# Kernel optimization log

Measured on AMD Instinct MI355X. Metric: run time of the kernel, lower is better.

The kernel has to match this reference:

```python
import jax, jax.numpy as jnp
import numpy as np
from jax import lax

B, T, U, V = 4, 256, 64, 1024   # batch, enc frames, max target len, vocab (blank=0)
F, H, HD, J = 80, 512, 512, 512  # feat dim, enc dim, dec dim, joint dim
NEG = -1e30


def setup_inputs() -> dict:
    key = jax.random.key(0)
    ks = jax.random.split(key, 10)
    inputs = jax.random.normal(ks[0], (B, T, F), dtype=jnp.float32)
    targets = jax.random.randint(ks[1], (B, U), 1, V, dtype=jnp.int32)  # labels exclude blank=0
    input_lengths = jax.random.randint(ks[2], (B,), T // 2, T + 1, dtype=jnp.int32)
    target_lengths = jax.random.randint(ks[3], (B,), U // 2, U + 1, dtype=jnp.int32)
    s = 0.02
    W_enc = jax.random.normal(ks[4], (F, H), dtype=jnp.float32) * s
    emb = jax.random.normal(ks[5], (V, HD), dtype=jnp.float32) * s
    W_jenc = jax.random.normal(ks[6], (H, J), dtype=jnp.float32) * s
    W_jdec = jax.random.normal(ks[7], (HD, J), dtype=jnp.float32) * s
    b_j = jnp.zeros((J,), dtype=jnp.float32)
    W_out = jax.random.normal(ks[8], (J, V), dtype=jnp.float32) * s
    b_out = jnp.zeros((V,), dtype=jnp.float32)
    return {"inputs": inputs, "W_enc": W_enc, "emb": emb, "W_jenc": W_jenc,
            "W_jdec": W_jdec, "b_j": b_j, "W_out": W_out, "b_out": b_out,
            "targets": targets, "input_lengths": input_lengths,
            "target_lengths": target_lengths}


def rnnt_loss(log_probs, targets, in_lens, tgt_lens):
    """RNN-T loss (blank=0, 'gather' variant: gather blank/label lps, then DP).
    log_probs: (B,T,U+1,V) log-softmaxed joint. Returns mean loss over batch."""
    Bq, Tq, U1, _ = log_probs.shape
    Uq = U1 - 1
    blank_lp = log_probs[..., 0]                                    # (B,T,U+1)
    lbl_lp = jnp.take_along_axis(
        log_probs[:, :, :Uq, :],
        jnp.broadcast_to(targets[:, None, :, None], (Bq, Tq, Uq, 1)),
        axis=3)[..., 0]                                             # (B,T,U)
    u_idx = jnp.arange(Uq)
    lbl_lp = jnp.where(u_idx[None, None, :] < tgt_lens[:, None, None], lbl_lp, NEG)

    def row(a, py):
        # a: (B,U+1) = alpha_prev + blank emission; py: (B,U) label lps this frame
        def step(c, x):
            a_u, py_prev = x
            c = jnp.logaddexp(a_u, c + py_prev)
            return c, c
        c0 = a[:, 0]
        _, rest = lax.scan(step, c0, (a[:, 1:].T, py.T))            # (U,B)
        return jnp.concatenate([c0[:, None], rest.T], axis=1)      # (B,U+1)

    # t=0 row: alpha[0,u] = cumsum of label lps at frame 0
    alpha0 = jnp.concatenate(
        [jnp.zeros((Bq, 1), log_probs.dtype),
         jnp.cumsum(lbl_lp[:, 0, :], axis=1)], axis=1)              # (B,U+1)

    def tstep(alpha_prev, x):
        blank_prev, py_t = x
        alpha = row(alpha_prev + blank_prev, py_t)
        return alpha, alpha

    xs = (jnp.swapaxes(blank_lp[:, :-1, :], 0, 1),                  # (T-1,B,U+1)
          jnp.swapaxes(lbl_lp[:, 1:, :], 0, 1))                    # (T-1,B,U)
    _, rest = lax.scan(tstep, alpha0, xs)
    alphas = jnp.concatenate([alpha0[None], rest], axis=0)          # (T,B,U+1)

    b = jnp.arange(Bq)
    t_last = in_lens - 1
    a_fin = alphas[t_last, b, tgt_lens] + blank_lp[b, t_last, tgt_lens]
    return -jnp.mean(a_fin)


def reference(inputs, W_enc, emb, W_jenc, W_jdec, b_j, W_out, b_out,
              targets, input_lengths, target_lengths):
    enc = inputs @ W_enc                                            # (B,T,H) encoder
    padded = jnp.concatenate(
        [jnp.zeros((targets.shape[0], 1), targets.dtype), targets], axis=1)
    dec = emb[padded]                                               # (B,U+1,HD) decoder
    e = enc @ W_jenc                                                # (B,T,J)
    d = dec @ W_jdec                                                # (B,U+1,J)
    h = jnp.tanh(e[:, :, None, :] + d[:, None, :, :] + b_j)        # (B,T,U+1,J)
    logits = h @ W_out + b_out                                      # (B,T,U+1,V)
    log_probs = jax.nn.log_softmax(logits, axis=-1)
    return rnnt_loss(log_probs, targets, input_lengths, target_lengths)
```

## Files before the change

### kernel.cpp

```cpp
#include <hip/hip_runtime.h>
#include <stdint.h>

#define NEGF (-1e30f)

typedef unsigned short ushort_t;
typedef unsigned char uchar_t;
typedef __attribute__((ext_vector_type(2))) long v2i64;
typedef __attribute__((ext_vector_type(4))) float f32x4;

constexpr int cB = 4, cT = 256, cU = 64, cU1 = 65, cV = 1024, cF = 80, cH = 512, cJ = 512;
constexpr int cM = cB * cT * cU1;
constexpr int cTU = cT * cU1;
constexpr float LOG2E = 1.4426950408889634f;

__device__ __forceinline__ float tanh_fast(float x){
  float t = x * x;
  float num = x * (27.f + t);
  float den = fmaf(9.f, t, 27.f);
  float r = num * __builtin_amdgcn_rcpf(den);
  return fminf(1.f, fmaxf(-1.f, r));
}

__device__ __forceinline__ float logadd2(float x, float y){
  float m = fmaxf(x, y);
  return m + __builtin_amdgcn_logf(1.f + __builtin_amdgcn_exp2f(-fabsf(x - y)));
}

__device__ __forceinline__ float wshr1(float x){
  return __int_as_float(__builtin_amdgcn_mov_dpp(__float_as_int(x),
                                                 0x138, 0xF, 0xF, true));
}

__device__ __forceinline__ int pk8(float a, float b, float c, float d){
  int v = __builtin_amdgcn_cvt_pk_fp8_f32(a, b, 0, false);
  v = __builtin_amdgcn_cvt_pk_fp8_f32(c, d, v, true);
  return v;
}

__global__ __launch_bounds__(256) void k_pre(
    const float* __restrict__ inputs,
    const float* __restrict__ W_enc, const float* __restrict__ W_jenc,
    const float* __restrict__ emb, const int* __restrict__ targets,
    const float* __restrict__ W_jdec, const float* __restrict__ b_j,
    float* __restrict__ dmatb, float* __restrict__ e,
    const float* __restrict__ W_out, uchar_t* __restrict__ WTf8,
    float* __restrict__ S, float* __restrict__ out_loss)
{
  __shared__ float sA[4][512];
  __shared__ float sIn[4][80];
  int bid = blockIdx.x;
  int tid = threadIdx.x;

  if (bid < 256){
    int m0 = bid * 4;
    for (int i = tid; i < 320; i += 256)
      sIn[i / 80][i % 80] = inputs[m0 * 80 + i];
    __syncthreads();
    int c0 = tid, c1 = tid + 256;
    float a00 = 0.f, a01 = 0.f, a10 = 0.f, a11 = 0.f;
    float a20 = 0.f, a21 = 0.f, a30 = 0.f, a31 = 0.f;
#pragma unroll 8
    for (int k = 0; k < 80; k++){
      float w0 = W_enc[(size_t)k * 512 + c0];
      float w1 = W_enc[(size_t)k * 512 + c1];
      a00 = fmaf(sIn[0][k], w0, a00); a01 = fmaf(sIn[0][k], w1, a01);
      a10 = fmaf(sIn[1][k], w0, a10); a11 = fmaf(sIn[1][k], w1, a11);
      a20 = fmaf(sIn[2][k], w0, a20); a21 = fmaf(sIn[2][k], w1, a21);
      a30 = fmaf(sIn[3][k], w0, a30); a31 = fmaf(sIn[3][k], w1, a31);
    }
    sA[0][c0] = a00; sA[0][c1] = a01;
    sA[1][c0] = a10; sA[1][c1] = a11;
    sA[2][c0] = a20; sA[2][c1] = a21;
    sA[3][c0] = a30; sA[3][c1] = a31;
    __syncthreads();
    float b00 = 0.f, b01 = 0.f, b10 = 0.f, b11 = 0.f;
    float b20 = 0.f, b21 = 0.f, b30 = 0.f, b31 = 0.f;
#pragma unroll 8
    for (int k = 0; k < 512; k++){
      float w0 = W_jenc[(size_t)k * 512 + c0];
      float w1 = W_jenc[(size_t)k * 512 + c1];
      b00 = fmaf(sA[0][k], w0, b00); b01 = fmaf(sA[0][k], w1, b01);
      b10 = fmaf(sA[1][k], w0, b10); b11 = fmaf(sA[1][k], w1, b11);
      b20 = fmaf(sA[2][k], w0, b20); b21 = fmaf(sA[2][k], w1, b21);
      b30 = fmaf(sA[3][k], w0, b30); b31 = fmaf(sA[3][k], w1, b31);
    }
    e[(size_t)(m0 + 0) * 512 + c0] = b00; e[(size_t)(m0 + 0) * 512 + c1] = b01;
    e[(size_t)(m0 + 1) * 512 + c0] = b10; e[(size_t)(m0 + 1) * 512 + c1] = b11;
    e[(size_t)(m0 + 2) * 512 + c0] = b20; e[(size_t)(m0 + 2) * 512 + c1] = b21;
    e[(size_t)(m0 + 3) * 512 + c0] = b30; e[(size_t)(m0 + 3) * 512 + c1] = b31;
  } else if (bid < 386){
    int id = bid - 256;
    int bx = id & 1, by = id >> 1;
    int m0 = by * 4;
    int col = bx * 256 + tid;
    for (int i = tid; i < 4 * 512; i += 256){
      int r = i >> 9, c = i & 511;
      int row = m0 + r;
      int b = row / cU1, u = row % cU1;
      int src = (u == 0) ? 0 : targets[b * cU + (u - 1)];
      sA[r][c] = emb[(size_t)src * cH + c];
    }
    __syncthreads();
    float a0 = 0.f, a1 = 0.f, a2 = 0.f, a3 = 0.f;
#pragma unroll 8
    for (int k = 0; k < 512; k++){
      float bv = W_jdec[(size_t)k * cJ + col];
      a0 = fmaf(sA[0][k], bv, a0);
      a1 = fmaf(sA[1][k], bv, a1);
      a2 = fmaf(sA[2][k], bv, a2);
      a3 = fmaf(sA[3][k], bv, a3);
    }
    float bb = b_j[col];
    dmatb[(size_t)(m0 + 0) * cJ + col] = a0 + bb;
    dmatb[(size_t)(m0 + 1) * cJ + col] = a1 + bb;
    dmatb[(size_t)(m0 + 2) * cJ + col] = a2 + bb;
    dmatb[(size_t)(m0 + 3) * cJ + col] = a3 + bb;
  } else if (bid < 418){
    int id = bid - 386;
    int bn = id & 3, ksp = id >> 2;
    int lane = tid & 63, nth = tid >> 6;
    int c16 = lane & 15, quad = lane >> 4;
    int jA = ksp * 64 + quad * 8;
#pragma unroll
    for (int i = 0; i < 4; i++){
      int nt16 = nth * 4 + i;
      int n = bn * 256 + nt16 * 16 + c16;
      unsigned int p[4];
#pragma unroll
      for (int h = 0; h < 4; h++){
        int j0 = jA + (h >> 1) * 32 + (h & 1) * 4;
        float w0 = W_out[(size_t)(j0 + 0) * cV + n] * 32.f;
        float w1 = W_out[(size_t)(j0 + 1) * cV + n] * 32.f;
        float w2 = W_out[(size_t)(j0 + 2) * cV + n] * 32.f;
        float w3 = W_out[(size_t)(j0 + 3) * cV + n] * 32.f;
        p[h] = (unsigned)pk8(w0, w1, w2, w3);
      }
      uint4 pack; pack.x = p[0]; pack.y = p[1]; pack.z = p[2]; pack.w = p[3];
      *(uint4*)(WTf8 + (((size_t)(bn * 8 + ksp) * 16 + nt16) * 64 + lane) * 16) = pack;
    }
  } else {
    int i = (bid - 418) * 1024 + tid * 4;
    float4 z; z.x = 0.f; z.y = 0.f; z.z = 0.f; z.w = 0.f;
    *(float4*)(S + i) = z;
    if (bid == 418 && tid == 0) out_loss[0] = 0.f;
  }
}

__global__ __launch_bounds__(256) void k_hf(const float* __restrict__ e,
                                            const float* __restrict__ dmatb,
                                            uchar_t* __restrict__ Hbf8){
  __shared__ uchar_t sH[16 * 520];
  int tid = threadIdx.x;
  int wid = tid >> 6, lane = tid & 63;
  int c16 = lane & 15, quad = lane >> 4;
  int bm = blockIdx.x;
  int bu = bm >> 1, thalf = bm & 1;
  int b = bu / cU1;
  int t0 = thalf * 128;

  float dj[8];
  const float4* dp = (const float4*)(dmatb + (size_t)bu * cJ + lane * 8);
  float4 dA = dp[0], dB = dp[1];
  dj[0] = dA.x; dj[1] = dA.y; dj[2] = dA.z; dj[3] = dA.w;
  dj[4] = dB.x; dj[5] = dB.y; dj[6] = dB.z; dj[7] = dB.w;

  const float* erow0 = e + ((size_t)(b * cT + t0)) * cJ + lane * 8;
  uchar_t* outb = Hbf8 + (size_t)bm * 65536 + lane * 16;

  for (int mg = 0; mg < 8; mg++){
#pragma unroll
    for (int rr = 0; rr < 4; rr++){
      int rloc = wid * 4 + rr;
      const float* ep = erow0 + ((size_t)(mg * 16 + rloc)) * cJ;
      float4 e0 = *(const float4*)ep;
      float4 e1 = *(const float4*)(ep + 4);
      int v0 = pk8(tanh_fast(e0.x + dj[0]), tanh_fast(e0.y + dj[1]),
                   tanh_fast(e0.z + dj[2]), tanh_fast(e0.w + dj[3]));
      int v1 = pk8(tanh_fast(e1.x + dj[4]), tanh_fast(e1.y + dj[5]),
                   tanh_fast(e1.z + dj[6]), tanh_fast(e1.w + dj[7]));
      uint2 pk; pk.x = (unsigned)v0; pk.y = (unsigned)v1;
      *(uint2*)(sH + rloc * 520 + lane * 8) = pk;
    }
    __syncthreads();
#pragma unroll
    for (int q = 0; q < 2; q++){
      int ksp = wid * 2 + q;
      uint2 lo = *(const uint2*)(sH + c16 * 520 + ksp * 64 + quad * 8);
      uint2 hi = *(const uint2*)(sH + c16 * 520 + ksp * 64 + 32 + quad * 8);
      uint4 pack; pack.x = lo.x; pack.y = lo.y; pack.z = hi.x; pack.w = hi.y;
      *(uint4*)(outb + ((size_t)ksp * 8 + mg) * 1024) = pack;
    }
    __syncthreads();
  }
}

__global__ __launch_bounds__(256, 3) void k_joint(
    const uchar_t* __restrict__ Hbf8, const uchar_t* __restrict__ WTf8,
    const float* __restrict__ b_out, const int* __restrict__ targets,
    float* __restrict__ S,
    float* __restrict__ blank_g, float* __restrict__ lbl_g)
{
  __shared__ float redP[2][128][19];

  int tid = threadIdx.x;
  int wid = tid >> 6, lane = tid & 63;
  int quad = lane >> 4, c16 = lane & 15;
  int wm = wid & 1, wn = wid >> 1;
  int bid = blockIdx.x;
  int bm = ((bid >> 6) << 3) + (bid & 7);
  int bn = (bid >> 3) & 7;
  int bu = bm >> 1, thalf = bm & 1;
  int b = bu / cU1, u = bu - b * cU1;
  int tg = (u < cU) ? targets[b * cU + u] : -1;
  int lin0 = bu * cT + thalf * 128;

  f32x4 acc[4][4];
#pragma unroll
  for (int i = 0; i < 4; i++)
#pragma unroll
    for (int j = 0; j < 4; j++)
      acc[i][j] = (f32x4){0.f, 0.f, 0.f, 0.f};

  const uchar_t* aP = Hbf8 + (size_t)bm * 65536 + (wm * 4) * 1024 + lane * 16;
  const uchar_t* bP = WTf8 + (size_t)(bn >> 1) * 131072 + ((bn & 1) * 8 + wn * 4) * 1024 + lane * 16;

  v2i64 afX[4], bfX[4], afY[4], bfY[4];
#pragma unroll
  for (int mt = 0; mt < 4; mt++) afX[mt] = *(const v2i64*)(aP + mt * 1024);
#pragma unroll
  for (int nt = 0; nt < 4; nt++) bfX[nt] = *(const v2i64*)(bP + nt * 1024);

#pragma unroll
  for (int k2 = 0; k2 < 4; k2++){
    {
      size_t kY = (size_t)(2 * k2 + 1);
#pragma unroll
      for (int mt = 0; mt < 4; mt++) afY[mt] = *(const v2i64*)(aP + kY * 8192 + mt * 1024);
#pragma unroll
      for (int nt = 0; nt < 4; nt++) bfY[nt] = *(const v2i64*)(bP + kY * 16384 + nt * 1024);
    }
#pragma unroll
    for (int h = 0; h < 2; h++)
#pragma unroll
      for (int mt = 0; mt < 4; mt++)
#pragma unroll
        for (int nt = 0; nt < 4; nt++)
          acc[mt][nt] = __builtin_amdgcn_mfma_f32_16x16x32_fp8_fp8(afX[mt][h], bfX[nt][h], acc[mt][nt], 0, 0, 0);
    if (k2 < 3){
      size_t kX = (size_t)(2 * k2 + 2);
#pragma unroll
      for (int mt = 0; mt < 4; mt++) afX[mt] = *(const v2i64*)(aP + kX * 8192 + mt * 1024);
#pragma unroll
      for (int nt = 0; nt < 4; nt++) bfX[nt] = *(const v2i64*)(bP + kX * 16384 + nt * 1024);
    }
#pragma unroll
    for (int h = 0; h < 2; h++)
#pragma unroll
      for (int mt = 0; mt < 4; mt++)
#pragma unroll
        for (int nt = 0; nt < 4; nt++)
          acc[mt][nt] = __builtin_amdgcn_mfma_f32_16x16x32_fp8_fp8(afY[mt][h], bfY[nt][h], acc[mt][nt], 0, 0, 0);
  }

  float bv[4];
#pragma unroll
  for (int nt = 0; nt < 4; nt++) bv[nt] = b_out[bn * 128 + (wn * 4 + nt) * 16 + c16] * LOG2E;

  bool ownL = (tg >= 0) && ((tg >> 7) == bn) && (((tg >> 6) & 1) == wn);
  int ntO = (tg >> 4) & 3;
  int tgc = tg & 15;
  const float descale2 = LOG2E / 32.f;

#pragma unroll
  for (int mt = 0; mt < 4; mt++){
#pragma unroll
    for (int r = 0; r < 4; r++){
      int rl = wm * 64 + mt * 16 + quad * 4 + r;
      float l[4];
#pragma unroll
      for (int nt = 0; nt < 4; nt++) l[nt] = fmaf(acc[mt][nt][r], descale2, bv[nt]);
      if (bn == 0 && wn == 0 && c16 == 0) blank_g[lin0 + rl] = l[0];
      if (ownL && c16 == tgc){
        float v = l[0];
#pragma unroll
        for (int k = 1; k < 4; k++) v = (ntO == k) ? l[k] : v;
        lbl_g[lin0 + rl] = v;
      }
      redP[wn][rl][c16] = __builtin_amdgcn_exp2f(l[0]) + __builtin_amdgcn_exp2f(l[1])
                        + __builtin_amdgcn_exp2f(l[2]) + __builtin_amdgcn_exp2f(l[3]);
    }
  }
  __syncthreads();
  if (tid < 128){
    float a = 0.f;
#pragma unroll
    for (int j = 0; j < 16; j++) a += redP[0][tid][j] + redP[1][tid][j];
    atomicAdd(&S[lin0 + tid], a);
  }
}

__global__ __launch_bounds__(256) void k_dp(
    const float* __restrict__ S, const float* __restrict__ blank_g,
    const float* __restrict__ lbl_g,
    const int* __restrict__ in_len, const int* __restrict__ tgt_len,
    float* __restrict__ out)
{
  constexpr int G = 16;
  __shared__ float sbb[cTU];
  __shared__ float slb[cTU];
  __shared__ float sS[256];
  __shared__ float cC0[G * 64], cC1[G * 64], cC2[G * 64];
  __shared__ float cOA[G * 64], cOB[G * 64];
  int tid = threadIdx.x;
  int b = blockIdx.x;
  int tl  = tgt_len[b];
  size_t base = (size_t)b * cTU;
  for (int i = tid; i < cTU / 4; i += 256){
    int row = i >> 6;
    if (row > tl) continue;
    float4 sv = ((const float4*)(S + base))[i];
    float4 bvv = ((const float4*)(blank_g + base))[i];
    float4 ls;
    ls.x = __builtin_amdgcn_logf(sv.x); ls.y = __builtin_amdgcn_logf(sv.y);
    ls.z = __builtin_amdgcn_logf(sv.z); ls.w = __builtin_amdgcn_logf(sv.w);
    float4 bo;
    bo.x = bvv.x - ls.x; bo.y = bvv.y - ls.y;
    bo.z = bvv.z - ls.z; bo.w = bvv.w - ls.w;
    ((float4*)sbb)[i] = bo;
    float4 lo;
    if (row < tl){
      float4 lv = ((const float4*)(lbl_g + base))[i];
      lo.x = lv.x - ls.x; lo.y = lv.y - ls.y;
      lo.z = lv.z - ls.z; lo.w = lv.w - ls.w;
    } else {
      lo.x = NEGF; lo.y = NEGF; lo.z = NEGF; lo.w = NEGF;
    }
    ((float4*)slb)[i] = lo;
  }
  __syncthreads();

  int til = in_len[b] - 1;
  bool cap64 = (tl == 64);
  int u = tid;
  bool isTL = (u == tl);
  float fb = (tid < 64) ? sbb[(u << 8) + til] : 0.f;

  int need = til + tl;
  if (cap64 && til + 62 > need) need = til + 62;
  int gmax = (need >> 1) + 2;
  if (gmax > 159) gmax = 159;
  int nph = (gmax + G - 1) / G;

  float A = (u == 0) ? 0.f : NEGF;
  float res = 0.f;

  auto ld = [&](const float* p, int i, bool ok) -> float {
    float x = p[i & 255];
    return (ok & ((unsigned)i < 256u)) ? x : NEGF;
  };

  for (int p = 0; p < nph; p++){
    for (int w = tid; w < G * 64; w += 256){
      int gg = w >> 6, uu = w & 63;
      int g = p * G + gg;
      int i0 = 2 * g - uu;
      bool v1 = (uu >= 1), v2 = (uu >= 2);
      const float* pbu  = sbb + (uu << 8);
      const float* pbu1 = sbb + ((v1 ? uu - 1 : 0) << 8);
      const float* plu1 = slb + ((v1 ? uu - 1 : 0) << 8);
      const float* plu2 = slb + ((v2 ? uu - 2 : 0) << 8);
      float o0 = ld(pbu,  i0,     true);
      float o1 = ld(pbu,  i0 + 1, true);
      float o2 = ld(plu1, i0 + 1, v1);
      float o3 = ld(pbu1, i0 + 1, v1);
      float o4 = ld(plu1, i0 + 2, v1);
      float o5 = ld(plu2, i0 + 2, v2);
      cC0[w] = o0 + o1;
      cC1[w] = logadd2(o2 + o1, o3 + o4);
      cC2[w] = o5 + o4;
      cOA[w] = o0;
      cOB[w] = o2;
    }
    __syncthreads();
    if (tid < 64){
      float c0v = cC0[u], c1v = cC1[u], c2v = cC2[u];
      float oAv = cOA[u], oBv = cOB[u];
#pragma unroll
      for (int gg = 0; gg < G; gg++){
        int g = p * G + gg;
        int nx = (gg + 1 < G) ? ((gg + 1) << 6) + u : (gg << 6) + u;
        float nc0 = cC0[nx], nc1 = cC1[nx], nc2 = cC2[nx];
        float noA = cOA[nx], noB = cOB[nx];
        if (g < gmax){
          float up1 = wshr1(A);
          float up2 = wshr1(up1);
          int i0 = 2 * g - u;
          float Amid = logadd2(A + oAv, up1 + oBv);
          bool tv1 = ((unsigned)(i0 + 1) < 256u);
          Amid = tv1 ? Amid : NEGF;
          float a0 = A + c0v, a1 = up1 + c1v, a2 = up2 + c2v;
          float m3 = fmaxf(fmaxf(a0, a1), a2);
          float s3 = __builtin_amdgcn_exp2f(a0 - m3) + __builtin_amdgcn_exp2f(a1 - m3)
                   + __builtin_amdgcn_exp2f(a2 - m3);
          float Anew = m3 + __builtin_amdgcn_logf(s3);
          bool tv2 = ((unsigned)(i0 + 2) < 256u);
          Anew = tv2 ? Anew : NEGF;
          if (isTL && (i0 + 1) == til) res = Amid + fb;
          if (isTL && (i0 + 2) == til) res = Anew + fb;
          if (u == 63){
            if (tv1) sS[i0 + 1] = Amid;
            if (tv2) sS[i0 + 2] = Anew;
          }
          A = Anew;
        }
        c0v = nc0; c1v = nc1; c2v = nc2; oAv = noA; oBv = noB;
      }
    }
    __syncthreads();
  }

  if (tid >= 64) return;

  if (cap64){
    const float* pb64 = sbb + (64 << 8);
    const float* pl63 = slb + (63 << 8);
    float A64 = sS[0] + pl63[0];
    for (int t = 1; t <= til; t++)
      A64 = logadd2(A64 + pb64[t - 1], sS[t] + pl63[t]);
    if (u == 0) res = A64 + pb64[til];
  }

  res += __shfl_xor(res, 1, 64);
  res += __shfl_xor(res, 2, 64);
  res += __shfl_xor(res, 4, 64);
  res += __shfl_xor(res, 8, 64);
  res += __shfl_xor(res, 16, 64);
  res += __shfl_xor(res, 32, 64);
  if (u == 0) atomicAdd(out, -0.17328679513998632f * res);
}

extern "C" void kernel_launch(void* const* d_in, const int* in_sizes, int n_in,
                              void* d_out, int out_size, void* d_ws, size_t ws_size,
                              hipStream_t stream)
{
  (void)in_sizes; (void)n_in; (void)out_size; (void)ws_size;
  const float* inputs = (const float*)d_in[0];
  const float* W_enc  = (const float*)d_in[1];
  const float* emb    = (const float*)d_in[2];
  const float* W_jenc = (const float*)d_in[3];
  const float* W_jdec = (const float*)d_in[4];
  const float* b_j    = (const float*)d_in[5];
  const float* W_out  = (const float*)d_in[6];
  const float* b_out  = (const float*)d_in[7];
  const int* targets  = (const int*)d_in[8];
  const int* in_len   = (const int*)d_in[9];
  const int* tgt_len  = (const int*)d_in[10];

  char* w = (char*)d_ws;
  auto alloc = [&](size_t bytes){ char* p = w; w += (bytes + 255) & ~(size_t)255; return p; };
  float* e       = (float*)alloc((size_t)1024 * 512 * 4);
  float* dmatb   = (float*)alloc((size_t)260 * 512 * 4);
  float* blank_g = (float*)alloc((size_t)cM * 4);
  float* lbl_g   = (float*)alloc((size_t)cM * 4);
  float* S       = (float*)alloc((size_t)cM * 4);
  uchar_t* Hbf8  = (uchar_t*)alloc((size_t)520 * 65536);
  uchar_t* WTf8  = (uchar_t*)alloc((size_t)4 * 131072);

  k_pre<<<483, 256, 0, stream>>>(inputs, W_enc, W_jenc, emb, targets, W_jdec, b_j,
                                 dmatb, e, W_out, WTf8, S, (float*)d_out);
  k_hf<<<520, 256, 0, stream>>>(e, dmatb, Hbf8);
  k_joint<<<4160, 256, 0, stream>>>(Hbf8, WTf8, b_out, targets, S, blank_g, lbl_g);
  k_dp<<<4, 256, 0, stream>>>(S, blank_g, lbl_g, in_len, tgt_len, (float*)d_out);
}
```

Before: 202.9 us.

## Switch joint GEMM to 32x32x16 FP8 MFMA with matching operand layouts

Replaces the 16x16x32 FP8 MFMA tiles in the joint GEMM with 32x32x16 FP8 MFMA tiles, giving each wave a 2x2 grid of 32x32 accumulators instead of 4x4 grid of 16x16. The pre-packing of W_out and the tanh/pack kernel are rewritten to emit operands in the 32x32 fragment layout, and the epilogue row mapping and shared reduction buffer are widened to 32 columns. The aim is fewer MFMA issues and fewer fragment loads per K step. The cost is a larger LDS reduction buffer, more staging in k_hf, and a different accumulator register layout that could affect occupancy.

```diff
diff --git a/kernel.cpp b/kernel.cpp
--- a/kernel.cpp
+++ b/kernel.cpp
@@ -7,6 +7,7 @@
 typedef unsigned char uchar_t;
 typedef __attribute__((ext_vector_type(2))) long v2i64;
 typedef __attribute__((ext_vector_type(4))) float f32x4;
+typedef __attribute__((ext_vector_type(16))) float f32x16;
 
 constexpr int cB = 4, cT = 256, cU = 64, cU1 = 65, cV = 1024, cF = 80, cH = 512, cJ = 512;
 constexpr int cM = cB * cT * cU1;
@@ -117,26 +118,30 @@
     dmatb[(size_t)(m0 + 3) * cJ + col] = a3 + bb;
   } else if (bid < 418){
     int id = bid - 386;
-    int bn = id & 3, ksp = id >> 2;
-    int lane = tid & 63, nth = tid >> 6;
-    int c16 = lane & 15, quad = lane >> 4;
-    int jA = ksp * 64 + quad * 8;
-#pragma unroll
-    for (int i = 0; i < 4; i++){
-      int nt16 = nth * 4 + i;
-      int n = bn * 256 + nt16 * 16 + c16;
-      unsigned int p[4];
-#pragma unroll
-      for (int h = 0; h < 4; h++){
-        int j0 = jA + (h >> 1) * 32 + (h & 1) * 4;
-        float w0 = W_out[(size_t)(j0 + 0) * cV + n] * 32.f;
-        float w1 = W_out[(size_t)(j0 + 1) * cV + n] * 32.f;
-        float w2 = W_out[(size_t)(j0 + 2) * cV + n] * 32.f;
-        float w3 = W_out[(size_t)(j0 + 3) * cV + n] * 32.f;
-        p[h] = (unsigned)pk8(w0, w1, w2, w3);
+    int bn = id & 7, jq = id >> 3;
+    int lane = tid & 63, nt32 = tid >> 6;
+    int c32 = lane & 31, kh = lane >> 5;
+    int col = bn * 128 + nt32 * 32 + c32;
+#pragma unroll
+    for (int jj = 0; jj < 4; jj++){
+      int j = jq * 4 + jj;
+      unsigned p[4];
+#pragma unroll
+      for (int h = 0; h < 2; h++){
+        int k0 = 32 * j + 16 * h + kh * 8;
+        float w0 = W_out[(size_t)(k0 + 0) * cV + col] * 32.f;
+        float w1 = W_out[(size_t)(k0 + 1) * cV + col] * 32.f;
+        float w2 = W_out[(size_t)(k0 + 2) * cV + col] * 32.f;
+        float w3 = W_out[(size_t)(k0 + 3) * cV + col] * 32.f;
+        float w4 = W_out[(size_t)(k0 + 4) * cV + col] * 32.f;
+        float w5 = W_out[(size_t)(k0 + 5) * cV + col] * 32.f;
+        float w6 = W_out[(size_t)(k0 + 6) * cV + col] * 32.f;
+        float w7 = W_out[(size_t)(k0 + 7) * cV + col] * 32.f;
+        p[h * 2 + 0] = (unsigned)pk8(w0, w1, w2, w3);
+        p[h * 2 + 1] = (unsigned)pk8(w4, w5, w6, w7);
       }
       uint4 pack; pack.x = p[0]; pack.y = p[1]; pack.z = p[2]; pack.w = p[3];
-      *(uint4*)(WTf8 + (((size_t)(bn * 8 + ksp) * 16 + nt16) * 64 + lane) * 16) = pack;
+      *(uint4*)(WTf8 + (((size_t)(bn * 4 + nt32) * 16 + j) * 64 + lane) * 16) = pack;
     }
   } else {
     int i = (bid - 418) * 1024 + tid * 4;
@@ -149,10 +154,10 @@
 __global__ __launch_bounds__(256) void k_hf(const float* __restrict__ e,
                                             const float* __restrict__ dmatb,
                                             uchar_t* __restrict__ Hbf8){
-  __shared__ uchar_t sH[16 * 520];
+  __shared__ uchar_t sH[32 * 520];
   int tid = threadIdx.x;
   int wid = tid >> 6, lane = tid & 63;
-  int c16 = lane & 15, quad = lane >> 4;
+  int c32 = lane & 31, kh = lane >> 5;
   int bm = blockIdx.x;
   int bu = bm >> 1, thalf = bm & 1;
   int b = bu / cU1;
@@ -167,11 +172,11 @@
   const float* erow0 = e + ((size_t)(b * cT + t0)) * cJ + lane * 8;
   uchar_t* outb = Hbf8 + (size_t)bm * 65536 + lane * 16;
 
-  for (int mg = 0; mg < 8; mg++){
-#pragma unroll
-    for (int rr = 0; rr < 4; rr++){
-      int rloc = wid * 4 + rr;
-      const float* ep = erow0 + ((size_t)(mg * 16 + rloc)) * cJ;
+  for (int g = 0; g < 4; g++){
+#pragma unroll
+    for (int rr = 0; rr < 8; rr++){
+      int rloc = wid * 8 + rr;
+      const float* ep = erow0 + ((size_t)(g * 32 + rloc)) * cJ;
       float4 e0 = *(const float4*)ep;
       float4 e1 = *(const float4*)(ep + 4);
       int v0 = pk8(tanh_fast(e0.x + dj[0]), tanh_fast(e0.y + dj[1]),
@@ -183,12 +188,13 @@
     }
     __syncthreads();
 #pragma unroll
-    for (int q = 0; q < 2; q++){
-      int ksp = wid * 2 + q;
-      uint2 lo = *(const uint2*)(sH + c16 * 520 + ksp * 64 + quad * 8);
-      uint2 hi = *(const uint2*)(sH + c16 * 520 + ksp * 64 + 32 + quad * 8);
+    for (int jj = 0; jj < 4; jj++){
+      int j = wid * 4 + jj;
+      const uchar_t* src = sH + c32 * 520 + 32 * j + kh * 8;
+      uint2 lo = *(const uint2*)(src);
+      uint2 hi = *(const uint2*)(src + 16);
       uint4 pack; pack.x = lo.x; pack.y = lo.y; pack.z = hi.x; pack.w = hi.y;
-      *(uint4*)(outb + ((size_t)ksp * 8 + mg) * 1024) = pack;
+      *(uint4*)(outb + ((size_t)(g * 16 + j)) * 1024) = pack;
     }
     __syncthreads();
   }
@@ -200,11 +206,11 @@
     float* __restrict__ S,
     float* __restrict__ blank_g, float* __restrict__ lbl_g)
 {
-  __shared__ float redP[2][128][19];
+  __shared__ float redP[2][128][33];
 
   int tid = threadIdx.x;
   int wid = tid >> 6, lane = tid & 63;
-  int quad = lane >> 4, c16 = lane & 15;
+  int c32 = lane & 31, kh = lane >> 5;
   int wm = wid & 1, wn = wid >> 1;
   int bid = blockIdx.x;
   int bm = ((bid >> 6) << 3) + (bid & 7);
@@ -214,87 +220,81 @@
   int tg = (u < cU) ? targets[b * cU + u] : -1;
   int lin0 = bu * cT + thalf * 128;
 
-  f32x4 acc[4][4];
-#pragma unroll
-  for (int i = 0; i < 4; i++)
-#pragma unroll
-    for (int j = 0; j < 4; j++)
-      acc[i][j] = (f32x4){0.f, 0.f, 0.f, 0.f};
-
-  const uchar_t* aP = Hbf8 + (size_t)bm * 65536 + (wm * 4) * 1024 + lane * 16;
-  const uchar_t* bP = WTf8 + (size_t)(bn >> 1) * 131072 + ((bn & 1) * 8 + wn * 4) * 1024 + lane * 16;
-
-  v2i64 afX[4], bfX[4], afY[4], bfY[4];
-#pragma unroll
-  for (int mt = 0; mt < 4; mt++) afX[mt] = *(const v2i64*)(aP + mt * 1024);
-#pragma unroll
-  for (int nt = 0; nt < 4; nt++) bfX[nt] = *(const v2i64*)(bP + nt * 1024);
-
-#pragma unroll
-  for (int k2 = 0; k2 < 4; k2++){
+  f32x16 acc[2][2];
+#pragma unroll
+  for (int i = 0; i < 2; i++)
+#pragma unroll
+    for (int j = 0; j < 2; j++)
+#pragma unroll
+      for (int r = 0; r < 16; r++) acc[i][j][r] = 0.f;
+
+  const uchar_t* aP = Hbf8 + (size_t)bm * 65536 + (size_t)wm * 32768 + lane * 16;
+  const uchar_t* bP = WTf8 + (size_t)bn * 65536 + (size_t)wn * 32768 + lane * 16;
+
+  v2i64 afX[2], bfX[2], afY[2], bfY[2];
+#pragma unroll
+  for (int mt = 0; mt < 2; mt++) afX[mt] = *(const v2i64*)(aP + mt * 16384);
+#pragma unroll
+  for (int nt = 0; nt < 2; nt++) bfX[nt] = *(const v2i64*)(bP + nt * 16384);
+
+#pragma unroll
+  for (int j2 = 0; j2 < 8; j2++){
     {
-      size_t kY = (size_t)(2 * k2 + 1);
-#pragma unroll
-      for (int mt = 0; mt < 4; mt++) afY[mt] = *(const v2i64*)(aP + kY * 8192 + mt * 1024);
-#pragma unroll
-      for (int nt = 0; nt < 4; nt++) bfY[nt] = *(const v2i64*)(bP + kY * 16384 + nt * 1024);
+      size_t jY = (size_t)(2 * j2 + 1) * 1024;
+      afY[0] = *(const v2i64*)(aP + jY);
+      afY[1] = *(const v2i64*)(aP + 16384 + jY);
+      bfY[0] = *(const v2i64*)(bP + jY);
+      bfY[1] = *(const v2i64*)(bP + 16384 + jY);
     }
 #pragma unroll
     for (int h = 0; h < 2; h++)
 #pragma unroll
-      for (int mt = 0; mt < 4; mt++)
-#pragma unroll
-        for (int nt = 0; nt < 4; nt++)
-          acc[mt][nt] = __builtin_amdgcn_mfma_f32_16x16x32_fp8_fp8(afX[mt][h], bfX[nt][h], acc[mt][nt], 0, 0, 0);
-    if (k2 < 3){
-      size_t kX = (size_t)(2 * k2 + 2);
-#pragma unroll
-      for (int mt = 0; mt < 4; mt++) afX[mt] = *(const v2i64*)(aP + kX * 8192 + mt * 1024);
-#pragma unroll
-      for (int nt = 0; nt < 4; nt++) bfX[nt] = *(const v2i64*)(bP + kX * 16384 + nt * 1024);
+      for (int mt = 0; mt < 2; mt++)
+#pragma unroll
+        for (int nt = 0; nt < 2; nt++)
+          acc[mt][nt] = __builtin_amdgcn_mfma_f32_32x32x16_fp8_fp8(afX[mt][h], bfX[nt][h], acc[mt][nt], 0, 0, 0);
+    if (j2 < 7){
+      size_t jX = (size_t)(2 * j2 + 2) * 1024;
+      afX[0] = *(const v2i64*)(aP + jX);
+      afX[1] = *(const v2i64*)(aP + 16384 + jX);
+      bfX[0] = *(const v2i64*)(bP + jX);
+      bfX[1] = *(const v2i64*)(bP + 16384 + jX);
     }
 #pragma unroll
     for (int h = 0; h < 2; h++)
 #pragma unroll
-      for (int mt = 0; mt < 4; mt++)
-#pragma unroll
-        for (int nt = 0; nt < 4; nt++)
-          acc[mt][nt] = __builtin_amdgcn_mfma_f32_16x16x32_fp8_fp8(afY[mt][h], bfY[nt][h], acc[mt][nt], 0, 0, 0);
-  }
-
-  float bv[4];
-#pragma unroll
-  for (int nt = 0; nt < 4; nt++) bv[nt] = b_out[bn * 128 + (wn * 4 + nt) * 16 + c16] * LOG2E;
+      for (int mt = 0; mt < 2; mt++)
+#pragma unroll
+        for (int nt = 0; nt < 2; nt++)
+          acc[mt][nt] = __builtin_amdgcn_mfma_f32_32x32x16_fp8_fp8(afY[mt][h], bfY[nt][h], acc[mt][nt], 0, 0, 0);
+  }
+
+  float bv[2];
+#pragma unroll
+  for (int nt = 0; nt < 2; nt++) bv[nt] = b_out[bn * 128 + wn * 64 + nt * 32 + c32] * LOG2E;
 
   bool ownL = (tg >= 0) && ((tg >> 7) == bn) && (((tg >> 6) & 1) == wn);
-  int ntO = (tg >> 4) & 3;
-  int tgc = tg & 15;
+  int ntO = (tg >> 5) & 1;
+  int tgc = tg & 31;
   const float descale2 = LOG2E / 32.f;
 
 #pragma unroll
-  for (int mt = 0; mt < 4; mt++){
-#pragma unroll
-    for (int r = 0; r < 4; r++){
-      int rl = wm * 64 + mt * 16 + quad * 4 + r;
-      float l[4];
-#pragma unroll
-      for (int nt = 0; nt < 4; nt++) l[nt] = fmaf(acc[mt][nt][r], descale2, bv[nt]);
-      if (bn == 0 && wn == 0 && c16 == 0) blank_g[lin0 + rl] = l[0];
-      if (ownL && c16 == tgc){
-        float v = l[0];
-#pragma unroll
-        for (int k = 1; k < 4; k++) v = (ntO == k) ? l[k] : v;
-        lbl_g[lin0 + rl] = v;
-      }
-      redP[wn][rl][c16] = __builtin_amdgcn_exp2f(l[0]) + __builtin_amdgcn_exp2f(l[1])
-                        + __builtin_amdgcn_exp2f(l[2]) + __builtin_amdgcn_exp2f(l[3]);
+  for (int mt = 0; mt < 2; mt++){
+#pragma unroll
+    for (int r = 0; r < 16; r++){
+      int rl = wm * 64 + mt * 32 + (r & 3) + 8 * (r >> 2) + 4 * kh;
+      float l0 = fmaf(acc[mt][0][r], descale2, bv[0]);
+      float l1 = fmaf(acc[mt][1][r], descale2, bv[1]);
+      if (bn == 0 && wn == 0 && c32 == 0) blank_g[lin0 + rl] = l0;
+      if (ownL && c32 == tgc) lbl_g[lin0 + rl] = (ntO == 0) ? l0 : l1;
+      redP[wn][rl][c32] = __builtin_amdgcn_exp2f(l0) + __builtin_amdgcn_exp2f(l1);
     }
   }
   __syncthreads();
   if (tid < 128){
     float a = 0.f;
 #pragma unroll
-    for (int j = 0; j < 16; j++) a += redP[0][tid][j] + redP[1][tid][j];
+    for (int j = 0; j < 32; j++) a += redP[0][tid][j] + redP[1][tid][j];
     atomicAdd(&S[lin0 + tid], a);
   }
 }
@@ -464,7 +464,7 @@
   float* lbl_g   = (float*)alloc((size_t)cM * 4);
   float* S       = (float*)alloc((size_t)cM * 4);
   uchar_t* Hbf8  = (uchar_t*)alloc((size_t)520 * 65536);
-  uchar_t* WTf8  = (uchar_t*)alloc((size_t)4 * 131072);
+  uchar_t* WTf8  = (uchar_t*)alloc((size_t)8 * 65536);
 
   k_pre<<<483, 256, 0, stream>>>(inputs, W_enc, W_jenc, emb, targets, W_jdec, b_j,
                                  dmatb, e, W_out, WTf8, S, (float*)d_out);
```

Measured after the change: 222.4 us. 9.6% more time.
